# Optimization experiments

Measured on AMD Instinct MI355X. Metric: run time of the kernel, lower is better.

Reference implementation:

```python
import jax, jax.numpy as jnp
import numpy as np

# dims: T tokens, E experts, D model dim, F ffn dim, C per-expert capacity, K top-k routing
T, E, D, F, C, K = 4096, 8, 1024, 4096, 1536, 2


def setup_inputs() -> dict:
    key = jax.random.key(0)
    k_x, k_lg, k_w1, k_w2 = jax.random.split(key, 4)
    x = jax.random.normal(k_x, (T, D), jnp.float32)
    # external router: top-K of logits per token, softmax weights over kept logits
    logits = jax.random.normal(k_lg, (T, E), jnp.float32)
    topv, topi = jax.lax.top_k(logits, K)                      # (T,K)
    rows = jnp.arange(T)[:, None]
    route_mask = jnp.zeros((T, E), bool).at[rows, topi].set(True)
    route_weight = jnp.zeros((T, E), jnp.float32).at[rows, topi].set(
        jax.nn.softmax(topv, axis=-1))
    # stacked homogeneous expert MLP params (E leading axis, as in _stack_group)
    W1 = jax.random.normal(k_w1, (E, D, F), jnp.float32) / np.sqrt(D)
    b1 = jnp.zeros((E, F), jnp.float32)
    W2 = jax.random.normal(k_w2, (E, F, D), jnp.float32) / np.sqrt(F)
    b2 = jnp.zeros((E, D), jnp.float32)
    return dict(x=x, route_mask=route_mask, route_weight=route_weight,
                W1=W1, b1=b1, W2=W2, b2=b2)


def reference(x, route_mask, route_weight, W1, b1, W2, b2):
    """MoE with per-expert capacity: top-C tokens per expert by route weight,
    gather -> vmapped expert MLP -> weighted scatter-combine.
    Math identical to the one-hot slot einsums ('ect,t...->ec...' dispatch and
    'ecf,ect,te->tf' combine) of the original, expressed as gather/scatter.
    """
    Tn, En = route_mask.shape
    w_te = jnp.where(route_mask, route_weight, 0.0)            # (T,E)
    # per-expert scores; unrouted tokens get -inf so they can never be selected
    w_et = jnp.where(route_mask.T, w_te.T, -jnp.inf)           # (E,T)
    vals, idx = jax.lax.top_k(w_et, C)                         # (E,C) token ids per slot
    valid = jnp.isfinite(vals)                                  # slot actually filled
    # dispatch: gather token features into (E,C,D); empty slots are zero rows
    xe = x[idx] * valid[..., None]
    # grouped expert MLP (vmap over E via batched einsum)
    h = jax.nn.relu(jnp.einsum('ecd,edf->ecf', xe, W1) + b1[:, None, :])
    out = jnp.einsum('ecf,efd->ecd', h, W2) + b2[:, None, :]    # (E,C,D)
    # combine: y[t] = sum over slots assigned to t of w_te[t,e] * out[e,c]
    gain = jnp.where(valid, jnp.take_along_axis(w_te.T, idx, axis=1), 0.0)  # (E,C)
    y = jnp.zeros((Tn, out.shape[-1]), out.dtype)
    y = y.at[idx.reshape(-1)].add((out * gain[..., None]).reshape(-1, out.shape[-1]))
    return y
```

## Files before the change

### kernel.cpp

```cpp
#include <hip/hip_runtime.h>
#include <hip/hip_bf16.h>
#include <stdint.h>

#define T_TOK 4096
#define NE    8
#define DM    1024
#define FF    4096
#define CAP   1536

typedef __attribute__((ext_vector_type(8))) __bf16 bf16x8;
typedef __attribute__((ext_vector_type(4))) float  f32x4;

__device__ __forceinline__ void gload_lds16(const void* gptr, void* lptr) {
  __builtin_amdgcn_global_load_lds(
      (__attribute__((address_space(1))) void*)(uintptr_t)gptr,
      (__attribute__((address_space(3))) void*)(uintptr_t)lptr,
      16, 0, 0);
}


__global__ void conv_x_kernel(const float4* __restrict__ src, ushort4* __restrict__ dst, int n4) {
  int i = blockIdx.x * blockDim.x + threadIdx.x;
  if (i >= n4) return;
  float4 v = src[i];
  ushort4 o;
  o.x = __builtin_bit_cast(unsigned short, __float2bfloat16(v.x));
  o.y = __builtin_bit_cast(unsigned short, __float2bfloat16(v.y));
  o.z = __builtin_bit_cast(unsigned short, __float2bfloat16(v.z));
  o.w = __builtin_bit_cast(unsigned short, __float2bfloat16(v.w));
  dst[i] = o;
}

__global__ void tconv_kernel(const float* __restrict__ src, __hip_bfloat16* __restrict__ dst,
                             int R, int C) {
  __shared__ float tile[32][33];
  const int b  = blockIdx.z;
  const int r0 = blockIdx.y * 32;
  const int c0 = blockIdx.x * 32;
  const float* s = src + (size_t)b * R * C;
  __hip_bfloat16* d = dst + (size_t)b * R * C;
  const int tx = threadIdx.x, ty = threadIdx.y;
#pragma unroll
  for (int rr = ty; rr < 32; rr += 8)
    tile[rr][tx] = s[(size_t)(r0 + rr) * C + c0 + tx];
  __syncthreads();
#pragma unroll
  for (int cc = ty; cc < 32; cc += 8)
    d[(size_t)(c0 + cc) * R + r0 + tx] = __float2bfloat16(tile[tx][cc]);
}

__global__ void router_kernel(const float* __restrict__ rw, int* __restrict__ counts,
                              int* __restrict__ tok_ids, float* __restrict__ gains) {
  int t = blockIdx.x * blockDim.x + threadIdx.x;
  if (t >= T_TOK) return;
#pragma unroll
  for (int e = 0; e < NE; ++e) {
    float w = rw[t * NE + e];
    if (w > 0.f) {
      int pos = atomicAdd(&counts[e], 1);
      if (pos < CAP) {
        tok_ids[e * CAP + pos] = t;
        gains[e * CAP + pos]   = w;
      }
    }
  }
}

__global__ void pad_kernel(const int* __restrict__ counts, int* __restrict__ tok_ids,
                           float* __restrict__ gains) {
  int i = blockIdx.x * blockDim.x + threadIdx.x;
  if (i >= NE * CAP) return;
  int e = i / CAP, pos = i % CAP;
  int ne = min(counts[e], CAP);
  if (pos >= ne) { tok_ids[i] = 0; gains[i] = 0.f; }
}


template <int PASS>
__global__ __launch_bounds__(256, 2)
void moe_gemm(const __hip_bfloat16* __restrict__ Asrc,
              const __hip_bfloat16* __restrict__ Bsrc,
              const float* __restrict__ bias,
              const int* __restrict__ counts,
              const int* __restrict__ tok_ids,
              const float* __restrict__ gains,
              __hip_bfloat16* __restrict__ Hout,
              float* __restrict__ y)
{
  constexpr int K  = (PASS == 1) ? DM : FF;
  constexpr int NP = (PASS == 1) ? FF : DM;
  constexpr int MT = CAP / 128;
  constexpr int NT = NP / 128;

  const int bid = blockIdx.x;
  const int e   = bid / (MT * NT);
  const int rem = bid % (MT * NT);
  const int mt  = rem / NT;
  const int nt  = rem % NT;

  const int Ne = min(counts[e], CAP);
  const int m0 = mt * 128;
  if (m0 >= Ne) return;
  const int n0 = nt * 128;

  __shared__ alignas(16) __hip_bfloat16 As[128 * 32];
  __shared__ alignas(16) __hip_bfloat16 Bs[128 * 32];

  const int tid  = threadIdx.x;
  const int lane = tid & 63;
  const int wid  = tid >> 6;
  const int wm   = wid >> 1;
  const int wn   = wid & 1;

  const int srow0 = tid >> 2;
  const int srow1 = 64 + (tid >> 2);
  const int schk  = (tid & 3) * 8;

  const __hip_bfloat16 *aptr0, *aptr1;
  if (PASS == 1) {
    const int tok0 = tok_ids[e * CAP + m0 + srow0];
    const int tok1 = tok_ids[e * CAP + m0 + srow1];
    aptr0 = Asrc + (size_t)tok0 * DM + schk;
    aptr1 = Asrc + (size_t)tok1 * DM + schk;
  } else {
    aptr0 = Asrc + ((size_t)e * CAP + m0 + srow0) * FF + schk;
    aptr1 = Asrc + ((size_t)e * CAP + m0 + srow1) * FF + schk;
  }
  const __hip_bfloat16* bptr0 = Bsrc + ((size_t)e * NP + n0 + srow0) * K + schk;
  const __hip_bfloat16* bptr1 = Bsrc + ((size_t)e * NP + n0 + srow1) * K + schk;

  char* asw0 = (char*)As + wid * 1024;
  char* asw1 = (char*)As + 4096 + wid * 1024;
  char* bsw0 = (char*)Bs + wid * 1024;
  char* bsw1 = (char*)Bs + 4096 + wid * 1024;

  const char* AsB = (const char*)As;
  const char* BsB = (const char*)Bs;
  const int fr = lane & 15;
  const int fq = lane >> 4;
  const int koffB = fq * 16;

  f32x4 acc[4][4] = {};

  for (int k0 = 0; k0 < K; k0 += 32) {
    gload_lds16(aptr0, asw0);
    gload_lds16(aptr1, asw1);
    gload_lds16(bptr0, bsw0);
    gload_lds16(bptr1, bsw1);
    aptr0 += 32; aptr1 += 32; bptr0 += 32; bptr1 += 32;
    __syncthreads();

    bf16x8 af[4], bfr[4];
#pragma unroll
    for (int i = 0; i < 4; ++i)
      af[i] = *(const bf16x8*)(AsB + (wm * 64 + i * 16 + fr) * 64 + koffB);
#pragma unroll
    for (int j = 0; j < 4; ++j)
      bfr[j] = *(const bf16x8*)(BsB + (wn * 64 + j * 16 + fr) * 64 + koffB);
#pragma unroll
    for (int i = 0; i < 4; ++i)
#pragma unroll
      for (int j = 0; j < 4; ++j)
        acc[i][j] = __builtin_amdgcn_mfma_f32_16x16x32_bf16(af[i], bfr[j], acc[i][j], 0, 0, 0);
    __syncthreads();
  }

  const int colb = n0 + wn * 64 + fr;
  if (PASS == 1) {
#pragma unroll
    for (int j = 0; j < 4; ++j) {
      const float bv = bias[(size_t)e * NP + colb + j * 16];
#pragma unroll
      for (int i = 0; i < 4; ++i)
#pragma unroll
        for (int rr = 0; rr < 4; ++rr) {
          const int row = m0 + wm * 64 + i * 16 + fq * 4 + rr;
          float v = acc[i][j][rr] + bv;
          v = v > 0.f ? v : 0.f;
          Hout[((size_t)e * CAP + row) * FF + colb + j * 16] = __float2bfloat16(v);
        }
    }
  } else {
    float bv[4];
#pragma unroll
    for (int j = 0; j < 4; ++j) bv[j] = bias[(size_t)e * NP + colb + j * 16];
#pragma unroll
    for (int i = 0; i < 4; ++i)
#pragma unroll
      for (int rr = 0; rr < 4; ++rr) {
        const int row  = m0 + wm * 64 + i * 16 + fq * 4 + rr;
        const int slot = e * CAP + row;
        const float g  = gains[slot];
        if (g != 0.f) {
          const int tok = tok_ids[slot];
          float* yrow = y + (size_t)tok * DM + colb;
#pragma unroll
          for (int j = 0; j < 4; ++j)
            atomicAdd(yrow + j * 16, (acc[i][j][rr] + bv[j]) * g);
        }
      }
  }
}


extern "C" void kernel_launch(void* const* d_in, const int* in_sizes, int n_in,
                              void* d_out, int out_size, void* d_ws, size_t ws_size,
                              hipStream_t stream) {
  const float* x  = (const float*)d_in[0];
  const float* rw = (const float*)d_in[2];
  const float* W1 = (const float*)d_in[3];
  const float* b1 = (const float*)d_in[4];
  const float* W2 = (const float*)d_in[5];
  const float* b2 = (const float*)d_in[6];
  float* y = (float*)d_out;

  char* ws = (char*)d_ws;
  size_t off = 0;
  auto alloc = [&](size_t bytes) {
    void* p = ws + off;
    off = (off + bytes + 255) & ~(size_t)255;
    return p;
  };
  __hip_bfloat16* xb  = (__hip_bfloat16*)alloc((size_t)T_TOK * DM * 2);
  __hip_bfloat16* w1t = (__hip_bfloat16*)alloc((size_t)NE * DM * FF * 2);
  __hip_bfloat16* w2t = (__hip_bfloat16*)alloc((size_t)NE * FF * DM * 2);
  __hip_bfloat16* Hb  = (__hip_bfloat16*)alloc((size_t)NE * CAP * FF * 2);
  int*   counts  = (int*)alloc(NE * sizeof(int));
  int*   tok_ids = (int*)alloc((size_t)NE * CAP * sizeof(int));
  float* gains   = (float*)alloc((size_t)NE * CAP * sizeof(float));
  (void)ws_size; (void)in_sizes; (void)n_in; (void)out_size;

  hipMemsetAsync(y, 0, (size_t)T_TOK * DM * sizeof(float), stream);
  hipMemsetAsync(counts, 0, NE * sizeof(int), stream);

  conv_x_kernel<<<(T_TOK * DM / 4 + 255) / 256, 256, 0, stream>>>(
      (const float4*)x, (ushort4*)xb, T_TOK * DM / 4);
  tconv_kernel<<<dim3(FF / 32, DM / 32, NE), dim3(32, 8), 0, stream>>>(W1, w1t, DM, FF);
  tconv_kernel<<<dim3(DM / 32, FF / 32, NE), dim3(32, 8), 0, stream>>>(W2, w2t, FF, DM);
  router_kernel<<<(T_TOK + 255) / 256, 256, 0, stream>>>(rw, counts, tok_ids, gains);
  pad_kernel<<<(NE * CAP + 255) / 256, 256, 0, stream>>>(counts, tok_ids, gains);

  moe_gemm<1><<<NE * (CAP / 128) * (FF / 128), 256, 0, stream>>>(
      xb, w1t, b1, counts, tok_ids, gains, Hb, nullptr);
  moe_gemm<2><<<NE * (CAP / 128) * (DM / 128), 256, 0, stream>>>(
      Hb, w2t, b2, counts, tok_ids, gains, nullptr, y);
}
```

Baseline: 390.2 us.

## Double-buffer MoE GEMM LDS with swizzle and widen transpose tiles

The expert GEMM now double-buffers its LDS tiles, issuing the next K-slice's global-to-LDS loads before computing the current one, with explicit vmcnt waits and barriers. An XOR swizzle on the 16-byte column chunks is meant to reduce LDS bank conflicts on fragment reads. The occupancy hint is raised to 3 blocks per SM. The weight transpose/convert kernel moves to 64x64 tiles with 4-wide bf16 stores to improve write coalescing. The cost is doubled LDS per block and possible register pressure from the higher occupancy target.

```diff
diff --git a/kernel.cpp b/kernel.cpp
--- a/kernel.cpp
+++ b/kernel.cpp
@@ -31,22 +31,34 @@
   dst[i] = o;
 }
 
-__global__ void tconv_kernel(const float* __restrict__ src, __hip_bfloat16* __restrict__ dst,
-                             int R, int C) {
-  __shared__ float tile[32][33];
+__global__ __launch_bounds__(256)
+void tconv_kernel(const float* __restrict__ src, __hip_bfloat16* __restrict__ dst,
+                  int R, int C) {
+  __shared__ float tile[64][65];
   const int b  = blockIdx.z;
-  const int r0 = blockIdx.y * 32;
-  const int c0 = blockIdx.x * 32;
+  const int r0 = blockIdx.y * 64;
+  const int c0 = blockIdx.x * 64;
   const float* s = src + (size_t)b * R * C;
   __hip_bfloat16* d = dst + (size_t)b * R * C;
-  const int tx = threadIdx.x, ty = threadIdx.y;
-#pragma unroll
-  for (int rr = ty; rr < 32; rr += 8)
+  const int tid = threadIdx.x;
+  const int tx = tid & 63, ty = tid >> 6;
+#pragma unroll
+  for (int rr = ty; rr < 64; rr += 4)
     tile[rr][tx] = s[(size_t)(r0 + rr) * C + c0 + tx];
   __syncthreads();
-#pragma unroll
-  for (int cc = ty; cc < 32; cc += 8)
-    d[(size_t)(c0 + cc) * R + r0 + tx] = __float2bfloat16(tile[tx][cc]);
+  const int lg = tid & 15;
+  const int cg = tid >> 4;
+#pragma unroll
+  for (int w = 0; w < 4; ++w) {
+    const int cc = w * 16 + cg;
+    const int r4 = lg * 4;
+    ushort4 o;
+    o.x = __builtin_bit_cast(unsigned short, __float2bfloat16(tile[r4 + 0][cc]));
+    o.y = __builtin_bit_cast(unsigned short, __float2bfloat16(tile[r4 + 1][cc]));
+    o.z = __builtin_bit_cast(unsigned short, __float2bfloat16(tile[r4 + 2][cc]));
+    o.w = __builtin_bit_cast(unsigned short, __float2bfloat16(tile[r4 + 3][cc]));
+    *(ushort4*)&d[(size_t)(c0 + cc) * R + r0 + r4] = o;
+  }
 }
 
 __global__ void router_kernel(const float* __restrict__ rw, int* __restrict__ counts,
@@ -77,7 +89,7 @@
 
 
 template <int PASS>
-__global__ __launch_bounds__(256, 2)
+__global__ __launch_bounds__(256, 3)
 void moe_gemm(const __hip_bfloat16* __restrict__ Asrc,
               const __hip_bfloat16* __restrict__ Bsrc,
               const float* __restrict__ bias,
@@ -91,6 +103,7 @@
   constexpr int NP = (PASS == 1) ? FF : DM;
   constexpr int MT = CAP / 128;
   constexpr int NT = NP / 128;
+  constexpr int KT = K / 32;
 
   const int bid = blockIdx.x;
   const int e   = bid / (MT * NT);
@@ -103,8 +116,8 @@
   if (m0 >= Ne) return;
   const int n0 = nt * 128;
 
-  __shared__ alignas(16) __hip_bfloat16 As[128 * 32];
-  __shared__ alignas(16) __hip_bfloat16 Bs[128 * 32];
+  __shared__ alignas(16) __hip_bfloat16 As[2 * 128 * 32];
+  __shared__ alignas(16) __hip_bfloat16 Bs[2 * 128 * 32];
 
   const int tid  = threadIdx.x;
   const int lane = tid & 63;
@@ -112,58 +125,72 @@
   const int wm   = wid >> 1;
   const int wn   = wid & 1;
 
-  const int srow0 = tid >> 2;
-  const int srow1 = 64 + (tid >> 2);
-  const int schk  = (tid & 3) * 8;
+  const int srow  = tid >> 2;
+  const int cs    = ((tid & 3) ^ ((srow >> 1) & 3)) * 8;
 
   const __hip_bfloat16 *aptr0, *aptr1;
   if (PASS == 1) {
-    const int tok0 = tok_ids[e * CAP + m0 + srow0];
-    const int tok1 = tok_ids[e * CAP + m0 + srow1];
-    aptr0 = Asrc + (size_t)tok0 * DM + schk;
-    aptr1 = Asrc + (size_t)tok1 * DM + schk;
+    const int tok0 = tok_ids[e * CAP + m0 + srow];
+    const int tok1 = tok_ids[e * CAP + m0 + 64 + srow];
+    aptr0 = Asrc + (size_t)tok0 * DM + cs;
+    aptr1 = Asrc + (size_t)tok1 * DM + cs;
   } else {
-    aptr0 = Asrc + ((size_t)e * CAP + m0 + srow0) * FF + schk;
-    aptr1 = Asrc + ((size_t)e * CAP + m0 + srow1) * FF + schk;
-  }
-  const __hip_bfloat16* bptr0 = Bsrc + ((size_t)e * NP + n0 + srow0) * K + schk;
-  const __hip_bfloat16* bptr1 = Bsrc + ((size_t)e * NP + n0 + srow1) * K + schk;
-
-  char* asw0 = (char*)As + wid * 1024;
-  char* asw1 = (char*)As + 4096 + wid * 1024;
-  char* bsw0 = (char*)Bs + wid * 1024;
-  char* bsw1 = (char*)Bs + 4096 + wid * 1024;
-
-  const char* AsB = (const char*)As;
-  const char* BsB = (const char*)Bs;
+    aptr0 = Asrc + ((size_t)e * CAP + m0 + srow) * FF + cs;
+    aptr1 = Asrc + ((size_t)e * CAP + m0 + 64 + srow) * FF + cs;
+  }
+  const __hip_bfloat16* bptr0 = Bsrc + ((size_t)e * NP + n0 + srow) * K + cs;
+  const __hip_bfloat16* bptr1 = Bsrc + ((size_t)e * NP + n0 + 64 + srow) * K + cs;
+
+  char* AsB = (char*)As;
+  char* BsB = (char*)Bs;
   const int fr = lane & 15;
   const int fq = lane >> 4;
-  const int koffB = fq * 16;
+  const int kbyte = ((fq ^ ((fr >> 1) & 3)) << 4);
 
   f32x4 acc[4][4] = {};
 
-  for (int k0 = 0; k0 < K; k0 += 32) {
-    gload_lds16(aptr0, asw0);
-    gload_lds16(aptr1, asw1);
-    gload_lds16(bptr0, bsw0);
-    gload_lds16(bptr1, bsw1);
-    aptr0 += 32; aptr1 += 32; bptr0 += 32; bptr1 += 32;
-    __syncthreads();
-
-    bf16x8 af[4], bfr[4];
-#pragma unroll
-    for (int i = 0; i < 4; ++i)
-      af[i] = *(const bf16x8*)(AsB + (wm * 64 + i * 16 + fr) * 64 + koffB);
-#pragma unroll
-    for (int j = 0; j < 4; ++j)
-      bfr[j] = *(const bf16x8*)(BsB + (wn * 64 + j * 16 + fr) * 64 + koffB);
-#pragma unroll
-    for (int i = 0; i < 4; ++i)
-#pragma unroll
-      for (int j = 0; j < 4; ++j)
-        acc[i][j] = __builtin_amdgcn_mfma_f32_16x16x32_bf16(af[i], bfr[j], acc[i][j], 0, 0, 0);
-    __syncthreads();
-  }
+#define STAGE(buf, kt)                                                        \
+  do {                                                                        \
+    gload_lds16(aptr0 + (kt) * 32, AsB + (buf) * 8192 + wid * 1024);          \
+    gload_lds16(aptr1 + (kt) * 32, AsB + (buf) * 8192 + 4096 + wid * 1024);   \
+    gload_lds16(bptr0 + (kt) * 32, BsB + (buf) * 8192 + wid * 1024);          \
+    gload_lds16(bptr1 + (kt) * 32, BsB + (buf) * 8192 + 4096 + wid * 1024);   \
+  } while (0)
+
+#define COMPUTE(buf)                                                          \
+  do {                                                                        \
+    const char* Ab = AsB + (buf) * 8192;                                      \
+    const char* Bb = BsB + (buf) * 8192;                                      \
+    bf16x8 af[4], bfr[4];                                                     \
+    _Pragma("unroll") for (int i = 0; i < 4; ++i)                             \
+        af[i] = *(const bf16x8*)(Ab + (wm * 64 + i * 16 + fr) * 64 + kbyte);  \
+    _Pragma("unroll") for (int j = 0; j < 4; ++j)                             \
+        bfr[j] = *(const bf16x8*)(Bb + (wn * 64 + j * 16 + fr) * 64 + kbyte); \
+    _Pragma("unroll") for (int i = 0; i < 4; ++i)                             \
+        _Pragma("unroll") for (int j = 0; j < 4; ++j)                         \
+            acc[i][j] = __builtin_amdgcn_mfma_f32_16x16x32_bf16(              \
+                af[i], bfr[j], acc[i][j], 0, 0, 0);                           \
+  } while (0)
+
+  STAGE(0, 0);
+  int cur = 0;
+  for (int kt = 0; kt + 1 < KT; ++kt) {
+    STAGE(cur ^ 1, kt + 1);
+    asm volatile("s_waitcnt vmcnt(4)" ::: "memory");
+    __builtin_amdgcn_s_barrier();
+    __builtin_amdgcn_sched_barrier(0);
+    COMPUTE(cur);
+    asm volatile("" ::: "memory");
+    __builtin_amdgcn_s_barrier();
+    cur ^= 1;
+  }
+  asm volatile("s_waitcnt vmcnt(0)" ::: "memory");
+  __builtin_amdgcn_s_barrier();
+  __builtin_amdgcn_sched_barrier(0);
+  COMPUTE(cur);
+
+#undef STAGE
+#undef COMPUTE
 
   const int colb = n0 + wn * 64 + fr;
   if (PASS == 1) {
@@ -235,8 +262,8 @@
 
   conv_x_kernel<<<(T_TOK * DM / 4 + 255) / 256, 256, 0, stream>>>(
       (const float4*)x, (ushort4*)xb, T_TOK * DM / 4);
-  tconv_kernel<<<dim3(FF / 32, DM / 32, NE), dim3(32, 8), 0, stream>>>(W1, w1t, DM, FF);
-  tconv_kernel<<<dim3(DM / 32, FF / 32, NE), dim3(32, 8), 0, stream>>>(W2, w2t, FF, DM);
+  tconv_kernel<<<dim3(FF / 64, DM / 64, NE), 256, 0, stream>>>(W1, w1t, DM, FF);
+  tconv_kernel<<<dim3(DM / 64, FF / 64, NE), 256, 0, stream>>>(W2, w2t, FF, DM);
   router_kernel<<<(T_TOK + 255) / 256, 256, 0, stream>>>(rw, counts, tok_ids, gains);
   pad_kernel<<<(NE * CAP + 255) / 256, 256, 0, stream>>>(counts, tok_ids, gains);
 
```

After: 351.9 us. 9.8% less time.
